# Kernel optimization log

Measured on AMD Instinct MI355X. Metric: run time of the kernel, lower is better.

Reference implementation:

```python
import jax, jax.numpy as jnp
import numpy as np

NUM_KERNELS = 301
GAMMA = 10.0
SHIFT = float(np.log(2.0))


def shifted_softplus(x):
    return jax.nn.softplus(x) - SHIFT


def setup_inputs() -> dict:
    key = jax.random.key(0)
    k1, k2, k3, k4, k5, k6 = jax.random.split(key, 6)
    N, F, K = 768, 128, NUM_KERNELS
    x = jax.random.normal(k1, (N, F), dtype=jnp.float32)
    # positions scaled to span a realistic distance range vs centers in [0, 30]
    r = jax.random.uniform(k2, (N, 3), dtype=jnp.float32) * 10.0
    W1 = jax.random.normal(k3, (K, F), dtype=jnp.float32) * (1.0 / np.sqrt(K))
    b1 = jax.random.normal(k4, (F,), dtype=jnp.float32) * 0.01
    W2 = jax.random.normal(k5, (F, F), dtype=jnp.float32) * (1.0 / np.sqrt(F))
    b2 = jax.random.normal(k6, (F,), dtype=jnp.float32) * 0.01
    return {"x": x, "r": r, "W1": W1, "b1": b1, "W2": W2, "b2": b2}


def reference(x, r, W1, b1, W2, b2):
    # pairwise Euclidean distances, safe at the zero diagonal
    diff = r[:, None, :] - r[None, :, :]            # [N, N, 3]
    sq = jnp.sum(diff * diff, axis=-1)              # [N, N]
    d = jnp.where(sq > 0, jnp.sqrt(jnp.where(sq > 0, sq, 1.0)), 0.0)
    centers = jnp.linspace(0.0, 30.0, NUM_KERNELS, dtype=jnp.float32)  # [K]
    expanded = jnp.exp(-GAMMA * jnp.square(d[..., None] - centers))    # [N, N, K]
    h = shifted_softplus(expanded @ W1 + b1)        # [N, N, F]
    w = shifted_softplus(h @ W2 + b2)               # [N, N, F]
    o = jnp.einsum('jk,ijk->ik', x, w)              # [N, F]
    return o
```

## Files before the change

### kernel.cpp

```cpp
#include <hip/hip_runtime.h>

#define F        128
#define NN       768
#define KE       192
#define E_STRIDE 200
#define H_STRIDE 136
#define NT       48
#define NPAIR    (NT*(NT+1)/2)
#define NBLK     (NPAIR*2)

#define L2E 1.44269504f
#define LN2 0.69314718f

typedef __attribute__((ext_vector_type(8))) short short8;
typedef __attribute__((ext_vector_type(4))) float floatx4;

__device__ __forceinline__ unsigned short f2bf(float f) {
    union { float f; unsigned u; } v; v.f = f;
    return (unsigned short)((v.u + 0x8000u) >> 16);
}

__device__ __forceinline__ float ssp_zl(float zl2e) {
    float t = exp2f(zl2e);
    float u = __log2f(1.0f + t);
    return fmaf(LN2, u, -LN2);
}

__device__ __forceinline__ void pin(short8& v) { asm volatile("" : "+v"(v)); }

__global__ void prep_w(const float* __restrict__ W1, const float* __restrict__ W2,
                       unsigned short* __restrict__ W1s, unsigned short* __restrict__ W2s,
                       float* __restrict__ out) {
    int bid = blockIdx.x, tid = threadIdx.x;
    if (bid < 384) {
        out[bid * 256 + tid] = 0.0f;
        return;
    }
    __shared__ unsigned short lds[32 * 128];
    int slice = bid - 384;
    const float* Wsrc;
    unsigned short* Wdst;
    int ks;
    if (slice < 6) { Wsrc = W1; Wdst = W1s; ks = slice; }
    else           { Wsrc = W2; Wdst = W2s; ks = slice - 6; }
    #pragma unroll
    for (int e = 0; e < 16; ++e) {
        int li = e * 256 + tid;
        lds[li] = f2bf(Wsrc[ks * 4096 + li]);
    }
    __syncthreads();
    #pragma unroll
    for (int e = 0; e < 16; ++e) {
        int oi = e * 256 + tid;
        int t = oi & 7, lane = (oi >> 3) & 63, frag = oi >> 9;
        int k_l = (lane >> 4) * 8 + t;
        int n   = frag * 16 + (lane & 15);
        Wdst[ks * 4096 + oi] = lds[k_l * 128 + n];
    }
}

__global__ __launch_bounds__(256, 2) void cfconv_main(
    const float* __restrict__ x, const float* __restrict__ r,
    const float* __restrict__ b1, const float* __restrict__ b2,
    const unsigned short* __restrict__ W1s, const unsigned short* __restrict__ W2s,
    float* __restrict__ out)
{
    __shared__ __align__(16) unsigned short e_lds[64 * E_STRIDE];
    __shared__ __align__(16) unsigned short h_lds[64 * H_STRIDE];
    __shared__ float d_all[128];

    const int tid  = threadIdx.x;
    const int lane = tid & 63;
    const int wave = tid >> 6;
    const int quad = lane >> 4;
    const int l15  = lane & 15;

    const int bid  = blockIdx.x;
    const int half = bid & 1;
    int b = bid >> 1;
    int A = (int)((97.0f - sqrtf(9409.0f - 8.0f * (float)b)) * 0.5f);
    while ((A + 1) * (97 - (A + 1)) / 2 <= b) ++A;
    while (A * (97 - A) / 2 > b) --A;
    const int B = A + (b - A * (97 - A) / 2);
    const int Ai0 = A * 16, Bj0 = B * 16;
    const bool diag = (A == B);

    short8 w1f[6][2], w2f[4][2];
    #pragma unroll
    for (int ks = 0; ks < KE / 32; ++ks) {
        w1f[ks][0] = *(const short8*)&W1s[((ks*8 + wave*2 + 0) * 64 + lane) * 8];
        w1f[ks][1] = *(const short8*)&W1s[((ks*8 + wave*2 + 1) * 64 + lane) * 8];
    }
    #pragma unroll
    for (int ks = 0; ks < F / 32; ++ks) {
        w2f[ks][0] = *(const short8*)&W2s[((ks*8 + wave*2 + 0) * 64 + lane) * 8];
        w2f[ks][1] = *(const short8*)&W2s[((ks*8 + wave*2 + 1) * 64 + lane) * 8];
    }
    #pragma unroll
    for (int ks = 0; ks < 6; ++ks) { pin(w1f[ks][0]); pin(w1f[ks][1]); }
    #pragma unroll
    for (int ks = 0; ks < 4; ++ks) { pin(w2f[ks][0]); pin(w2f[ks][1]); }

    if (tid < 128) {
        int P = half * 128 + tid;
        int gi = Ai0 + (P >> 4), gj = Bj0 + (P & 15);
        float dx = r[gi*3+0] - r[gj*3+0];
        float dy = r[gi*3+1] - r[gj*3+1];
        float dz = r[gi*3+2] - r[gj*3+2];
        float sq = dx*dx + dy*dy + dz*dz;
        d_all[tid] = sq > 0.0f ? sqrtf(sq) : 0.0f;
    }

    {
        short8 z = 0;
        short8* p8 = (short8*)e_lds;
        for (int c = tid; c < (64 * E_STRIDE) / 8; c += 256) p8[c] = z;
    }

    const int c0 = wave * 32 + l15;
    const int c1 = c0 + 16;
    const float b1L0 = b1[c0] * L2E, b1L1 = b1[c1] * L2E;
    const float b2L0 = b2[c0] * L2E, b2L1 = b2[c1] * L2E;

    float xB0[4], xB1[4];
    #pragma unroll
    for (int rg = 0; rg < 4; ++rg) {
        int gj = Bj0 + quad * 4 + rg;
        xB0[rg] = x[gj * F + c0];
        xB1[rg] = x[gj * F + c1];
    }
    float oB0[4] = {0,0,0,0}, oB1[4] = {0,0,0,0};

    const int rq16 = 16 * ((l15 >> 2) & 3);

    __syncthreads();

    #pragma unroll
    for (int sl = 0; sl < 2; ++sl) {
        const int s = half * 2 + sl;

        {
            int kl = lane & 31;
            for (int rr = wave * 2 + (lane >> 5); rr < 64; rr += 8) {
                if (sl > 0) {
                    float dp = d_all[rr];
                    int kp = ((int)ceilf(dp * 10.0f - 13.0f)) & ~1;
                    kp = kp < 0 ? 0 : (kp > KE - 32 ? KE - 32 : kp);
                    e_lds[rr * E_STRIDE + kp + kl] = 0;
                }
                float d = d_all[sl * 64 + rr];
                int klo = ((int)ceilf(d * 10.0f - 13.0f)) & ~1;
                klo = klo < 0 ? 0 : (klo > KE - 32 ? KE - 32 : klo);
                int k = klo + kl;
                float t = fmaf(-0.1f, (float)k, d);
                float e = exp2f(t * t * (-10.0f * L2E));
                e_lds[rr * E_STRIDE + k] = f2bf(e);
            }
        }
        __syncthreads();

        floatx4 acc[4][2];
        #pragma unroll
        for (int mt = 0; mt < 4; ++mt) { acc[mt][0] = 0; acc[mt][1] = 0; }
        #pragma unroll
        for (int ks = 0; ks < KE / 32; ++ks) {
            short8 af[4];
            #pragma unroll
            for (int mt = 0; mt < 4; ++mt)
                af[mt] = *(const short8*)&e_lds[(mt*16 + l15) * E_STRIDE + ks*32 + quad*8];
            #pragma unroll
            for (int mt = 0; mt < 4; ++mt) {
                acc[mt][0] = __builtin_amdgcn_mfma_f32_16x16x32_bf16(af[mt], w1f[ks][0], acc[mt][0], 0, 0, 0);
                acc[mt][1] = __builtin_amdgcn_mfma_f32_16x16x32_bf16(af[mt], w1f[ks][1], acc[mt][1], 0, 0, 0);
            }
        }

        #pragma unroll
        for (int mt = 0; mt < 4; ++mt) {
            #pragma unroll
            for (int rg = 0; rg < 4; ++rg) {
                int row = mt*16 + quad*4 + rg;
                float h0 = ssp_zl(fmaf(acc[mt][0][rg], L2E, b1L0));
                float h1 = ssp_zl(fmaf(acc[mt][1][rg], L2E, b1L1));
                h_lds[row * H_STRIDE + ((c0 + 16*quad) & 127)] = f2bf(h0);
                h_lds[row * H_STRIDE + ((c1 + 16*quad) & 127)] = f2bf(h1);
            }
        }
        __syncthreads();

        floatx4 acc2[4][2];
        #pragma unroll
        for (int mt = 0; mt < 4; ++mt) { acc2[mt][0] = 0; acc2[mt][1] = 0; }
        #pragma unroll
        for (int ks = 0; ks < F / 32; ++ks) {
            int ko = (ks*32 + quad*8 + rq16) & 127;
            short8 af[4];
            #pragma unroll
            for (int mt = 0; mt < 4; ++mt)
                af[mt] = *(const short8*)&h_lds[(mt*16 + l15) * H_STRIDE + ko];
            #pragma unroll
            for (int mt = 0; mt < 4; ++mt) {
                acc2[mt][0] = __builtin_amdgcn_mfma_f32_16x16x32_bf16(af[mt], w2f[ks][0], acc2[mt][0], 0, 0, 0);
                acc2[mt][1] = __builtin_amdgcn_mfma_f32_16x16x32_bf16(af[mt], w2f[ks][1], acc2[mt][1], 0, 0, 0);
            }
        }

        float xA0[4], xA1[4];
        #pragma unroll
        for (int mt = 0; mt < 4; ++mt) {
            int gi = Ai0 + s*4 + mt;
            xA0[mt] = x[gi * F + c0];
            xA1[mt] = x[gi * F + c1];
        }
        float oA0[4] = {0,0,0,0}, oA1[4] = {0,0,0,0};
        #pragma unroll
        for (int mt = 0; mt < 4; ++mt) {
            #pragma unroll
            for (int rg = 0; rg < 4; ++rg) {
                float w0 = ssp_zl(fmaf(acc2[mt][0][rg], L2E, b2L0));
                float w1 = ssp_zl(fmaf(acc2[mt][1][rg], L2E, b2L1));
                oA0[mt] = fmaf(xB0[rg], w0, oA0[mt]);
                oA1[mt] = fmaf(xB1[rg], w1, oA1[mt]);
                if (!diag) {
                    oB0[rg] = fmaf(xA0[mt], w0, oB0[rg]);
                    oB1[rg] = fmaf(xA1[mt], w1, oB1[rg]);
                }
            }
        }
        #pragma unroll
        for (int mt = 0; mt < 4; ++mt) {
            oA0[mt] += __shfl_xor(oA0[mt], 16, 64); oA0[mt] += __shfl_xor(oA0[mt], 32, 64);
            oA1[mt] += __shfl_xor(oA1[mt], 16, 64); oA1[mt] += __shfl_xor(oA1[mt], 32, 64);
        }
        if (lane < 16) {
            #pragma unroll
            for (int mt = 0; mt < 4; ++mt) {
                int gi = Ai0 + s*4 + mt;
                atomicAdd(&out[gi * F + c0], oA0[mt]);
                atomicAdd(&out[gi * F + c1], oA1[mt]);
            }
        }
        if (sl == 0) __syncthreads();
    }

    if (!diag) {
        #pragma unroll
        for (int rg = 0; rg < 4; ++rg) {
            int gj = Bj0 + quad * 4 + rg;
            atomicAdd(&out[gj * F + c0], oB0[rg]);
            atomicAdd(&out[gj * F + c1], oB1[rg]);
        }
    }
}

extern "C" void kernel_launch(void* const* d_in, const int* in_sizes, int n_in,
                              void* d_out, int out_size, void* d_ws, size_t ws_size,
                              hipStream_t stream) {
    const float* x  = (const float*)d_in[0];
    const float* r  = (const float*)d_in[1];
    const float* W1 = (const float*)d_in[2];
    const float* b1 = (const float*)d_in[3];
    const float* W2 = (const float*)d_in[4];
    const float* b2 = (const float*)d_in[5];
    float* out = (float*)d_out;

    unsigned short* W1s = (unsigned short*)d_ws;
    unsigned short* W2s = W1s + KE * F;

    prep_w<<<394, 256, 0, stream>>>(W1, W2, W1s, W2s, out);
    cfconv_main<<<NBLK, 256, 0, stream>>>(x, r, b1, b2, W1s, W2s, out);
}
```

Before: 131.3 us.

## Split each tile pair into four blocks, alias h into e LDS, raise occupancy

Each block now handles one 64-row slice instead of two, which doubles the grid to NPAIR*4 blocks, and launch bounds rise to 4 blocks per SM. The h buffer now aliases the e buffer, with an extra barrier, which roughly halves LDS per block. Distances are computed inline, and zero-fill covers only the needed row region. The aim is better latency hiding through higher occupancy. The cost is that W1/W2 fragment loads and B-side atomics are duplicated across twice as many blocks, and register pressure must fit the tighter launch bound.

```diff
diff --git a/kernel.cpp b/kernel.cpp
--- a/kernel.cpp
+++ b/kernel.cpp
@@ -7,7 +7,7 @@
 #define H_STRIDE 136
 #define NT       48
 #define NPAIR    (NT*(NT+1)/2)
-#define NBLK     (NPAIR*2)
+#define NBLK     (NPAIR*4)
 
 #define L2E 1.44269504f
 #define LN2 0.69314718f
@@ -59,15 +59,14 @@
     }
 }
 
-__global__ __launch_bounds__(256, 2) void cfconv_main(
+__global__ __launch_bounds__(256, 4) void cfconv_main(
     const float* __restrict__ x, const float* __restrict__ r,
     const float* __restrict__ b1, const float* __restrict__ b2,
     const unsigned short* __restrict__ W1s, const unsigned short* __restrict__ W2s,
     float* __restrict__ out)
 {
     __shared__ __align__(16) unsigned short e_lds[64 * E_STRIDE];
-    __shared__ __align__(16) unsigned short h_lds[64 * H_STRIDE];
-    __shared__ float d_all[128];
+    unsigned short* h_lds = e_lds;
 
     const int tid  = threadIdx.x;
     const int lane = tid & 63;
@@ -75,9 +74,9 @@
     const int quad = lane >> 4;
     const int l15  = lane & 15;
 
-    const int bid  = blockIdx.x;
-    const int half = bid & 1;
-    int b = bid >> 1;
+    const int bid = blockIdx.x;
+    const int s   = bid & 3;
+    int b = bid >> 2;
     int A = (int)((97.0f - sqrtf(9409.0f - 8.0f * (float)b)) * 0.5f);
     while ((A + 1) * (97 - (A + 1)) / 2 <= b) ++A;
     while (A * (97 - A) / 2 > b) --A;
@@ -101,22 +100,6 @@
     #pragma unroll
     for (int ks = 0; ks < 4; ++ks) { pin(w2f[ks][0]); pin(w2f[ks][1]); }
 
-    if (tid < 128) {
-        int P = half * 128 + tid;
-        int gi = Ai0 + (P >> 4), gj = Bj0 + (P & 15);
-        float dx = r[gi*3+0] - r[gj*3+0];
-        float dy = r[gi*3+1] - r[gj*3+1];
-        float dz = r[gi*3+2] - r[gj*3+2];
-        float sq = dx*dx + dy*dy + dz*dz;
-        d_all[tid] = sq > 0.0f ? sqrtf(sq) : 0.0f;
-    }
-
-    {
-        short8 z = 0;
-        short8* p8 = (short8*)e_lds;
-        for (int c = tid; c < (64 * E_STRIDE) / 8; c += 256) p8[c] = z;
-    }
-
     const int c0 = wave * 32 + l15;
     const int c1 = c0 + 16;
     const float b1L0 = b1[c0] * L2E, b1L1 = b1[c1] * L2E;
@@ -129,120 +112,115 @@
         xB0[rg] = x[gj * F + c0];
         xB1[rg] = x[gj * F + c1];
     }
-    float oB0[4] = {0,0,0,0}, oB1[4] = {0,0,0,0};
+    float xA0[4], xA1[4];
+    #pragma unroll
+    for (int mt = 0; mt < 4; ++mt) {
+        int gi = Ai0 + s * 4 + mt;
+        xA0[mt] = x[gi * F + c0];
+        xA1[mt] = x[gi * F + c1];
+    }
+
+    {
+        const int kl = lane & 31;
+        const bool zlane = kl < 25;
+        short8 z = 0;
+        for (int rr = wave * 2 + (lane >> 5); rr < 64; rr += 8) {
+            int gi = Ai0 + s * 4 + (rr >> 4);
+            int gj = Bj0 + (rr & 15);
+            float dx = r[gi*3+0] - r[gj*3+0];
+            float dy = r[gi*3+1] - r[gj*3+1];
+            float dz = r[gi*3+2] - r[gj*3+2];
+            float sq = dx*dx + dy*dy + dz*dz;
+            float d  = sq > 0.0f ? sqrtf(sq) : 0.0f;
+            if (zlane) *(short8*)&e_lds[rr * E_STRIDE + kl * 8] = z;
+            int klo = ((int)ceilf(d * 10.0f - 13.0f)) & ~1;
+            klo = klo < 0 ? 0 : (klo > KE - 32 ? KE - 32 : klo);
+            int k = klo + kl;
+            float t = fmaf(-0.1f, (float)k, d);
+            float e = exp2f(t * t * (-10.0f * L2E));
+            e_lds[rr * E_STRIDE + k] = f2bf(e);
+        }
+    }
+    __syncthreads();
+
+    floatx4 acc[4][2];
+    #pragma unroll
+    for (int mt = 0; mt < 4; ++mt) { acc[mt][0] = 0; acc[mt][1] = 0; }
+    #pragma unroll
+    for (int ks = 0; ks < KE / 32; ++ks) {
+        short8 af[4];
+        #pragma unroll
+        for (int mt = 0; mt < 4; ++mt)
+            af[mt] = *(const short8*)&e_lds[(mt*16 + l15) * E_STRIDE + ks*32 + quad*8];
+        #pragma unroll
+        for (int mt = 0; mt < 4; ++mt) {
+            acc[mt][0] = __builtin_amdgcn_mfma_f32_16x16x32_bf16(af[mt], w1f[ks][0], acc[mt][0], 0, 0, 0);
+            acc[mt][1] = __builtin_amdgcn_mfma_f32_16x16x32_bf16(af[mt], w1f[ks][1], acc[mt][1], 0, 0, 0);
+        }
+    }
+    __syncthreads();
+
+    #pragma unroll
+    for (int mt = 0; mt < 4; ++mt) {
+        #pragma unroll
+        for (int rg = 0; rg < 4; ++rg) {
+            int row = mt*16 + quad*4 + rg;
+            float h0 = ssp_zl(fmaf(acc[mt][0][rg], L2E, b1L0));
+            float h1 = ssp_zl(fmaf(acc[mt][1][rg], L2E, b1L1));
+            h_lds[row * H_STRIDE + ((c0 + 16*quad) & 127)] = f2bf(h0);
+            h_lds[row * H_STRIDE + ((c1 + 16*quad) & 127)] = f2bf(h1);
+        }
+    }
+    __syncthreads();
 
     const int rq16 = 16 * ((l15 >> 2) & 3);
-
-    __syncthreads();
-
-    #pragma unroll
-    for (int sl = 0; sl < 2; ++sl) {
-        const int s = half * 2 + sl;
-
-        {
-            int kl = lane & 31;
-            for (int rr = wave * 2 + (lane >> 5); rr < 64; rr += 8) {
-                if (sl > 0) {
-                    float dp = d_all[rr];
-                    int kp = ((int)ceilf(dp * 10.0f - 13.0f)) & ~1;
-                    kp = kp < 0 ? 0 : (kp > KE - 32 ? KE - 32 : kp);
-                    e_lds[rr * E_STRIDE + kp + kl] = 0;
-                }
-                float d = d_all[sl * 64 + rr];
-                int klo = ((int)ceilf(d * 10.0f - 13.0f)) & ~1;
-                klo = klo < 0 ? 0 : (klo > KE - 32 ? KE - 32 : klo);
-                int k = klo + kl;
-                float t = fmaf(-0.1f, (float)k, d);
-                float e = exp2f(t * t * (-10.0f * L2E));
-                e_lds[rr * E_STRIDE + k] = f2bf(e);
+    floatx4 acc2[4][2];
+    #pragma unroll
+    for (int mt = 0; mt < 4; ++mt) { acc2[mt][0] = 0; acc2[mt][1] = 0; }
+    #pragma unroll
+    for (int ks = 0; ks < F / 32; ++ks) {
+        int ko = (ks*32 + quad*8 + rq16) & 127;
+        short8 af[4];
+        #pragma unroll
+        for (int mt = 0; mt < 4; ++mt)
+            af[mt] = *(const short8*)&h_lds[(mt*16 + l15) * H_STRIDE + ko];
+        #pragma unroll
+        for (int mt = 0; mt < 4; ++mt) {
+            acc2[mt][0] = __builtin_amdgcn_mfma_f32_16x16x32_bf16(af[mt], w2f[ks][0], acc2[mt][0], 0, 0, 0);
+            acc2[mt][1] = __builtin_amdgcn_mfma_f32_16x16x32_bf16(af[mt], w2f[ks][1], acc2[mt][1], 0, 0, 0);
+        }
+    }
+
+    float oA0[4], oA1[4], oB0[4] = {0,0,0,0}, oB1[4] = {0,0,0,0};
+    #pragma unroll
+    for (int mt = 0; mt < 4; ++mt) { oA0[mt] = 0; oA1[mt] = 0; }
+    #pragma unroll
+    for (int mt = 0; mt < 4; ++mt) {
+        #pragma unroll
+        for (int rg = 0; rg < 4; ++rg) {
+            float w0 = ssp_zl(fmaf(acc2[mt][0][rg], L2E, b2L0));
+            float w1 = ssp_zl(fmaf(acc2[mt][1][rg], L2E, b2L1));
+            oA0[mt] = fmaf(xB0[rg], w0, oA0[mt]);
+            oA1[mt] = fmaf(xB1[rg], w1, oA1[mt]);
+            if (!diag) {
+                oB0[rg] = fmaf(xA0[mt], w0, oB0[rg]);
+                oB1[rg] = fmaf(xA1[mt], w1, oB1[rg]);
             }
         }
-        __syncthreads();
-
-        floatx4 acc[4][2];
-        #pragma unroll
-        for (int mt = 0; mt < 4; ++mt) { acc[mt][0] = 0; acc[mt][1] = 0; }
-        #pragma unroll
-        for (int ks = 0; ks < KE / 32; ++ks) {
-            short8 af[4];
-            #pragma unroll
-            for (int mt = 0; mt < 4; ++mt)
-                af[mt] = *(const short8*)&e_lds[(mt*16 + l15) * E_STRIDE + ks*32 + quad*8];
-            #pragma unroll
-            for (int mt = 0; mt < 4; ++mt) {
-                acc[mt][0] = __builtin_amdgcn_mfma_f32_16x16x32_bf16(af[mt], w1f[ks][0], acc[mt][0], 0, 0, 0);
-                acc[mt][1] = __builtin_amdgcn_mfma_f32_16x16x32_bf16(af[mt], w1f[ks][1], acc[mt][1], 0, 0, 0);
-            }
-        }
-
+    }
+    #pragma unroll
+    for (int mt = 0; mt < 4; ++mt) {
+        oA0[mt] += __shfl_xor(oA0[mt], 16, 64); oA0[mt] += __shfl_xor(oA0[mt], 32, 64);
+        oA1[mt] += __shfl_xor(oA1[mt], 16, 64); oA1[mt] += __shfl_xor(oA1[mt], 32, 64);
+    }
+    if (lane < 16) {
         #pragma unroll
         for (int mt = 0; mt < 4; ++mt) {
-            #pragma unroll
-            for (int rg = 0; rg < 4; ++rg) {
-                int row = mt*16 + quad*4 + rg;
-                float h0 = ssp_zl(fmaf(acc[mt][0][rg], L2E, b1L0));
-                float h1 = ssp_zl(fmaf(acc[mt][1][rg], L2E, b1L1));
-                h_lds[row * H_STRIDE + ((c0 + 16*quad) & 127)] = f2bf(h0);
-                h_lds[row * H_STRIDE + ((c1 + 16*quad) & 127)] = f2bf(h1);
-            }
-        }
-        __syncthreads();
-
-        floatx4 acc2[4][2];
-        #pragma unroll
-        for (int mt = 0; mt < 4; ++mt) { acc2[mt][0] = 0; acc2[mt][1] = 0; }
-        #pragma unroll
-        for (int ks = 0; ks < F / 32; ++ks) {
-            int ko = (ks*32 + quad*8 + rq16) & 127;
-            short8 af[4];
-            #pragma unroll
-            for (int mt = 0; mt < 4; ++mt)
-                af[mt] = *(const short8*)&h_lds[(mt*16 + l15) * H_STRIDE + ko];
-            #pragma unroll
-            for (int mt = 0; mt < 4; ++mt) {
-                acc2[mt][0] = __builtin_amdgcn_mfma_f32_16x16x32_bf16(af[mt], w2f[ks][0], acc2[mt][0], 0, 0, 0);
-                acc2[mt][1] = __builtin_amdgcn_mfma_f32_16x16x32_bf16(af[mt], w2f[ks][1], acc2[mt][1], 0, 0, 0);
-            }
-        }
-
-        float xA0[4], xA1[4];
-        #pragma unroll
-        for (int mt = 0; mt < 4; ++mt) {
-            int gi = Ai0 + s*4 + mt;
-            xA0[mt] = x[gi * F + c0];
-            xA1[mt] = x[gi * F + c1];
-        }
-        float oA0[4] = {0,0,0,0}, oA1[4] = {0,0,0,0};
-        #pragma unroll
-        for (int mt = 0; mt < 4; ++mt) {
-            #pragma unroll
-            for (int rg = 0; rg < 4; ++rg) {
-                float w0 = ssp_zl(fmaf(acc2[mt][0][rg], L2E, b2L0));
-                float w1 = ssp_zl(fmaf(acc2[mt][1][rg], L2E, b2L1));
-                oA0[mt] = fmaf(xB0[rg], w0, oA0[mt]);
-                oA1[mt] = fmaf(xB1[rg], w1, oA1[mt]);
-                if (!diag) {
-                    oB0[rg] = fmaf(xA0[mt], w0, oB0[rg]);
-                    oB1[rg] = fmaf(xA1[mt], w1, oB1[rg]);
-                }
-            }
-        }
-        #pragma unroll
-        for (int mt = 0; mt < 4; ++mt) {
-            oA0[mt] += __shfl_xor(oA0[mt], 16, 64); oA0[mt] += __shfl_xor(oA0[mt], 32, 64);
-            oA1[mt] += __shfl_xor(oA1[mt], 16, 64); oA1[mt] += __shfl_xor(oA1[mt], 32, 64);
-        }
-        if (lane < 16) {
-            #pragma unroll
-            for (int mt = 0; mt < 4; ++mt) {
-                int gi = Ai0 + s*4 + mt;
-                atomicAdd(&out[gi * F + c0], oA0[mt]);
-                atomicAdd(&out[gi * F + c1], oA1[mt]);
-            }
-        }
-        if (sl == 0) __syncthreads();
-    }
-
+            int gi = Ai0 + s * 4 + mt;
+            atomicAdd(&out[gi * F + c0], oA0[mt]);
+            atomicAdd(&out[gi * F + c1], oA1[mt]);
+        }
+    }
     if (!diag) {
         #pragma unroll
         for (int rg = 0; rg < 4; ++rg) {
```

New measurement: 151.2 us. +15.1%, slower.
